# Performance work log

Hardware: AMD Instinct MI355X
Metric: run time of the kernel (lower is better)

The kernel has to match this reference:

```python
import jax, jax.numpy as jnp
from jax import lax
import numpy as np

B, T, C = 4, 1024, 1024
NH, HS = 16, 64
K, STRIDE = 32, 16
EPS = 1e-5


def _ln(x, w, b):
    m = jnp.mean(x, axis=-1, keepdims=True)
    v = jnp.mean((x - m) ** 2, axis=-1, keepdims=True)
    return (x - m) * lax.rsqrt(v + EPS) * w + b


def setup_inputs() -> dict:
    key = jax.random.key(0)
    ks = jax.random.split(key, 12)
    s = 0.02
    return {
        'x': jax.random.normal(ks[0], (B, T, C), jnp.float32),
        'c_attn_w': jax.random.normal(ks[1], (C, 3 * C), jnp.float32) * s,
        'c_attn_b': jnp.zeros((3 * C,), jnp.float32),
        'c_proj_w': jax.random.normal(ks[2], (C, C), jnp.float32) * s,
        'c_proj_b': jnp.zeros((C,), jnp.float32),
        'conv_w': jax.random.normal(ks[3], (HS, HS, K), jnp.float32) * s,  # OIH
        'conv_b': jnp.zeros((HS,), jnp.float32),
        'comp_ln_w': jnp.ones((HS,), jnp.float32),
        'comp_ln_b': jnp.zeros((HS,), jnp.float32),
        'ln_local_w': jnp.ones((C,), jnp.float32),
        'ln_local_b': jnp.zeros((C,), jnp.float32),
        'gate_w1': jax.random.normal(ks[4], (2 * C, C), jnp.float32) * s,
        'gate_b1': jnp.zeros((C,), jnp.float32),
        'gate_ln_w': jnp.ones((C,), jnp.float32),
        'gate_ln_b': jnp.zeros((C,), jnp.float32),
        'gate_w2': jax.random.normal(ks[5], (C, 2), jnp.float32) * s,
        'gate_b2': jnp.zeros((2,), jnp.float32),
    }


def _compress(h, conv_w, conv_b, comp_ln_w, comp_ln_b):
    # h: [B, nh, T, hs] -> [B, nh, num_blocks, hs]
    b, nh, t, hs = h.shape
    xr = h.transpose(0, 1, 3, 2).reshape(b * nh, hs, t)  # NCH
    co = lax.conv_general_dilated(xr, conv_w, (STRIDE,), 'VALID',
                                  dimension_numbers=('NCH', 'OIH', 'NCH'))
    co = co + conv_b[None, :, None]
    y = co.transpose(0, 2, 1)  # [B*nh, nb, hs]
    y = _ln(y, comp_ln_w, comp_ln_b)
    y = jax.nn.gelu(y, approximate=False)
    return y.reshape(b, nh, -1, hs)


def _attn(q, k, v, mask):
    # q:[B,nh,T,hs] k,v:[B,nh,Tk,hs], mask:[T,Tk] bool (True=keep)
    scale = 1.0 / jnp.sqrt(jnp.asarray(q.shape[-1], q.dtype))
    att = jnp.einsum('bhqd,bhkd->bhqk', q, k) * scale
    att = jnp.where(mask[None, None], att, jnp.finfo(att.dtype).min)
    att = jax.nn.softmax(att, axis=-1)
    return jnp.einsum('bhqk,bhkd->bhqd', att, v)


def reference(x, c_attn_w, c_attn_b, c_proj_w, c_proj_b, conv_w, conv_b,
              comp_ln_w, comp_ln_b, ln_local_w, ln_local_b,
              gate_w1, gate_b1, gate_ln_w, gate_ln_b, gate_w2, gate_b2):
    b, t, c = x.shape
    qkv = x @ c_attn_w + c_attn_b
    q, k, v = jnp.split(qkv, 3, axis=-1)
    q = q.reshape(b, t, NH, HS).transpose(0, 2, 1, 3)
    k = k.reshape(b, t, NH, HS).transpose(0, 2, 1, 3)
    v = v.reshape(b, t, NH, HS).transpose(0, 2, 1, 3)

    k_comp = _compress(k, conv_w, conv_b, comp_ln_w, comp_ln_b)
    v_comp = _compress(v, conv_w, conv_b, comp_ln_w, comp_ln_b)
    nb = k_comp.shape[2]

    # local branch: flash path with is_causal=True skips the window mask -> plain causal
    causal = jnp.tril(jnp.ones((t, t), bool))
    local = _attn(q, k, v, causal)
    local = local.transpose(0, 2, 1, 3).reshape(b, t, c)
    local_norm = _ln(local, ln_local_w, ln_local_b)

    # compressed branch: causal mask of shape [T, num_blocks], diagonal 0
    comp_mask = jnp.tril(jnp.ones((t, nb), bool), k=0)
    comp = _attn(q, k_comp, v_comp, comp_mask)
    comp = comp.transpose(0, 2, 1, 3).reshape(b, t, c)

    # gating from last-token features
    feats = jnp.concatenate([local_norm[:, -1, :], comp[:, -1, :]], axis=-1)  # [B, 2C]
    h = jax.nn.relu(_ln(feats @ gate_w1 + gate_b1, gate_ln_w, gate_ln_b))
    gates = jax.nn.softmax(h @ gate_w2 + gate_b2, axis=-1)  # [B, 2]
    g = gates[:, None, :]  # [B, 1, 2]
    combined = g[..., 0:1] * local_norm + g[..., 1:2] * comp

    return combined @ c_proj_w + c_proj_b
```

## Files before the change

### kernel.cpp

```cpp
#include <hip/hip_runtime.h>

using u16 = unsigned short;
using f32x4 = __attribute__((ext_vector_type(4))) float;
using s16x8 = __attribute__((ext_vector_type(8))) short;
using u16x4 = __attribute__((ext_vector_type(4))) unsigned short;

__device__ __forceinline__ u16 f2bf(float f) {
  unsigned u = __float_as_uint(f);
  return (u16)((u + 0x7FFFu + ((u >> 16) & 1u)) >> 16);
}

__device__ __forceinline__ f32x4 mfma16(s16x8 a, s16x8 b, f32x4 c) {
  return __builtin_amdgcn_mfma_f32_16x16x32_bf16(a, b, c, 0, 0, 0);
}

__device__ __forceinline__ void gld16(const void* g, void* l) {
  __builtin_amdgcn_global_load_lds(
      (const __attribute__((address_space(1))) unsigned int*)g,
      (__attribute__((address_space(3))) unsigned int*)l, 16, 0, 0);
}

__global__ __launch_bounds__(256) void cast_bf16(const float* __restrict__ in,
                                                 u16* __restrict__ out, int n4) {
  int i = blockIdx.x * 256 + threadIdx.x;
  if (i >= n4) return;
  f32x4 v = *(const f32x4*)(in + (size_t)i * 4);
  u16x4 o = {f2bf(v[0]), f2bf(v[1]), f2bf(v[2]), f2bf(v[3])};
  *(u16x4*)(out + (size_t)i * 4) = o;
}

__global__ __launch_bounds__(256) void cast_wfrag(const float* __restrict__ in,
                                                  u16* __restrict__ out) {
  int t = blockIdx.x * 256 + threadIdx.x;
  int c = t & 63, blk = t >> 6;
  int j = blk & 3, ic = blk >> 2;
  int lr = c >> 2, lg = c & 3;
  const float* src = in + (size_t)(j * 16 + lr) * 2048 + ic * 32 + lg * 8;
  f32x4 a = *(const f32x4*)(src);
  f32x4 b = *(const f32x4*)(src + 4);
  u16* dst = out + (size_t)t * 8;
  u16x4 o0 = {f2bf(a[0]), f2bf(a[1]), f2bf(a[2]), f2bf(a[3])};
  u16x4 o1 = {f2bf(b[0]), f2bf(b[1]), f2bf(b[2]), f2bf(b[3])};
  *(u16x4*)(dst) = o0;
  *(u16x4*)(dst + 4) = o1;
}

__global__ __launch_bounds__(256) void transpose_cast(const float* __restrict__ in,
                                                      u16* __restrict__ out,
                                                      int R, int C) {
  __shared__ float t[32][33];
  int bx = blockIdx.x, by = blockIdx.y;
  int tx = threadIdx.x & 31, ty = threadIdx.x >> 5;
#pragma unroll
  for (int r = 0; r < 4; r++) {
    int row = by * 32 + ty + r * 8;
    t[ty + r * 8][tx] = in[(size_t)row * C + bx * 32 + tx];
  }
  __syncthreads();
#pragma unroll
  for (int r = 0; r < 4; r++) {
    int orow = bx * 32 + ty + r * 8;
    out[(size_t)orow * R + by * 32 + tx] = f2bf(t[tx][ty + r * 8]);
  }
}

__device__ __forceinline__ void gemm_mainloop(const u16* A, const u16* Bt, int K,
                                              u16* As, u16* Bs, f32x4 acc[4][4]) {
  const int tid = threadIdx.x;
  const int row = tid >> 2, c16 = tid & 3;
  const int lane = tid & 63, wid = tid >> 6;
  const int wm = wid >> 1, wn = wid & 1, lg = lane >> 4, lr = lane & 15;
  const u16* ga = A + (size_t)row * K + c16 * 8;
  const u16* gb = Bt + (size_t)row * K + c16 * 8;
  const size_t rowskip = (size_t)64 * K;
  for (int k0 = 0; k0 < K; k0 += 32) {
    gld16(ga + k0, As + tid * 8);
    gld16(ga + rowskip + k0, As + 2048 + tid * 8);
    gld16(gb + k0, Bs + tid * 8);
    gld16(gb + rowskip + k0, Bs + 2048 + tid * 8);
    __syncthreads();
    s16x8 af[4], bfr[4];
#pragma unroll
    for (int i = 0; i < 4; i++)
      af[i] = *(const s16x8*)(As + (wm * 64 + i * 16 + lr) * 32 + lg * 8);
#pragma unroll
    for (int j = 0; j < 4; j++)
      bfr[j] = *(const s16x8*)(Bs + (wn * 64 + j * 16 + lr) * 32 + lg * 8);
#pragma unroll
    for (int i = 0; i < 4; i++)
#pragma unroll
      for (int j = 0; j < 4; j++) acc[i][j] = mfma16(af[i], bfr[j], acc[i][j]);
    __syncthreads();
  }
}

__global__ __launch_bounds__(256) void gemm_qkv(const u16* __restrict__ A,
                                                const u16* __restrict__ Bt,
                                                const float* __restrict__ bias,
                                                u16* __restrict__ qo, u16* __restrict__ ko,
                                                u16* __restrict__ kTo, u16* __restrict__ vTo) {
  __shared__ u16 As[4096];
  __shared__ u16 Bs[4096];
  int m0 = blockIdx.x * 128, n0 = blockIdx.y * 128;
  f32x4 acc[4][4] = {};
  gemm_mainloop(A + (size_t)m0 * 1024, Bt + (size_t)n0 * 1024, 1024, As, Bs, acc);
  int lane = threadIdx.x & 63, wid = threadIdx.x >> 6;
  int wm = wid >> 1, wn = wid & 1, lg = lane >> 4, lr = lane & 15;
#pragma unroll
  for (int i = 0; i < 4; i++) {
    int mb = m0 + wm * 64 + i * 16 + lg * 4;
    int b = mb >> 10, tb = mb & 1023;
#pragma unroll
    for (int j = 0; j < 4; j++) {
      int n = n0 + wn * 64 + j * 16 + lr;
      float bs = bias[n];
      int sel = n >> 10, hd = n & 1023, h = hd >> 6, d = hd & 63;
      int bh = b * 16 + h;
      u16 u0 = f2bf(acc[i][j][0] + bs), u1 = f2bf(acc[i][j][1] + bs);
      u16 u2 = f2bf(acc[i][j][2] + bs), u3 = f2bf(acc[i][j][3] + bs);
      if (sel == 0) {
        u16* qp = qo + ((size_t)bh << 16) + ((size_t)tb << 6) + d;
        qp[0] = u0; qp[64] = u1; qp[128] = u2; qp[192] = u3;
      } else if (sel == 1) {
        u16* kp = ko + ((size_t)bh << 16) + ((size_t)tb << 6) + d;
        kp[0] = u0; kp[64] = u1; kp[128] = u2; kp[192] = u3;
        u16x4 pk = {u0, u1, u2, u3};
        *(u16x4*)(kTo + ((size_t)(bh * 64 + d) << 10) + tb) = pk;
      } else {
        u16x4 pk = {u0, u1, u2, u3};
        *(u16x4*)(vTo + ((size_t)(bh * 64 + d) << 10) + tb) = pk;
      }
    }
  }
}

__global__ __launch_bounds__(256) void gemm_proj(const u16* __restrict__ A,
                                                 const u16* __restrict__ Bt,
                                                 const float* __restrict__ bias,
                                                 float* __restrict__ out) {
  __shared__ u16 As[4096];
  __shared__ u16 Bs[4096];
  int m0 = blockIdx.x * 128, n0 = blockIdx.y * 128;
  f32x4 acc[4][4] = {};
  gemm_mainloop(A + (size_t)m0 * 1024, Bt + (size_t)n0 * 1024, 1024, As, Bs, acc);
  int lane = threadIdx.x & 63, wid = threadIdx.x >> 6;
  int wm = wid >> 1, wn = wid & 1, lg = lane >> 4, lr = lane & 15;
#pragma unroll
  for (int i = 0; i < 4; i++) {
    int mb = m0 + wm * 64 + i * 16 + lg * 4;
#pragma unroll
    for (int j = 0; j < 4; j++) {
      int n = n0 + wn * 64 + j * 16 + lr;
      float bs = bias[n];
#pragma unroll
      for (int r = 0; r < 4; r++)
        out[(size_t)(mb + r) * 1024 + n] = acc[i][j][r] + bs;
    }
  }
}

__global__ __launch_bounds__(512, 2) void conv_comp(const u16* __restrict__ kT,
                                                    const u16* __restrict__ vT,
                                                    const u16* __restrict__ wfrag,
                                                    const float* __restrict__ cb,
                                                    const float* __restrict__ lnw,
                                                    const float* __restrict__ lnb,
                                                    u16* __restrict__ kcomp,
                                                    u16* __restrict__ vcompT) {
  __shared__ float red[4][64][16];
  int bh = blockIdx.x, sel = blockIdx.y;
  const u16* src = (sel ? vT : kT) + ((size_t)bh << 16);
  int tid = threadIdx.x, w = tid >> 6, lane = tid & 63, lg = lane >> 4, lr = lane & 15;
  int wq = w & 3, ichalf = w >> 2;
  f32x4 acc[4] = {};
  int arow = wq * 16 + lr;
  if (arow > 62) arow = 62;
  const u16* abase = src + (size_t)arow * 16 + lg * 8;
  const u16* wbase = wfrag + (size_t)(lr * 4 + lg) * 8;
  int ic0 = ichalf * 32;
#pragma unroll 8
  for (int ic = ic0; ic < ic0 + 32; ic++) {
    s16x8 a = *(const s16x8*)(abase + ic * 1024);
    const u16* wrow = wbase + (size_t)ic * 2048;
#pragma unroll
    for (int j = 0; j < 4; j++) {
      s16x8 bfr = *(const s16x8*)(wrow + j * 512);
      acc[j] = mfma16(a, bfr, acc[j]);
    }
  }
  if (w >= 4) {
#pragma unroll
    for (int j = 0; j < 4; j++)
#pragma unroll
      for (int r = 0; r < 4; r++) red[wq][lane][j * 4 + r] = acc[j][r];
  }
  __syncthreads();
  if (w >= 4) return;
#pragma unroll
  for (int j = 0; j < 4; j++)
#pragma unroll
    for (int r = 0; r < 4; r++) acc[j][r] += red[wq][lane][j * 4 + r];
  float lwv[4], lbv[4];
#pragma unroll
  for (int j = 0; j < 4; j++) {
    int oc = j * 16 + lr;
    float cbv = cb[oc];
    acc[j][0] += cbv; acc[j][1] += cbv; acc[j][2] += cbv; acc[j][3] += cbv;
    lwv[j] = lnw[oc]; lbv[j] = lnb[oc];
  }
#pragma unroll
  for (int r = 0; r < 4; r++) {
    float s = acc[0][r] + acc[1][r] + acc[2][r] + acc[3][r];
    float q = acc[0][r] * acc[0][r] + acc[1][r] * acc[1][r] +
              acc[2][r] * acc[2][r] + acc[3][r] * acc[3][r];
#pragma unroll
    for (int off = 1; off < 16; off <<= 1) {
      s += __shfl_xor(s, off);
      q += __shfl_xor(q, off);
    }
    float mean = s * (1.f / 64.f);
    float var = q * (1.f / 64.f) - mean * mean;
    float rstd = rsqrtf(fmaxf(var, 0.f) + 1e-5f);
    int op = wq * 16 + lg * 4 + r;
#pragma unroll
    for (int j = 0; j < 4; j++) {
      float y = (acc[j][r] - mean) * rstd * lwv[j] + lbv[j];
      y = 0.5f * y * (1.0f + erff(y * 0.70710678118f));
      if (op > 62) y = 0.f;
      int oc = j * 16 + lr;
      if (sel == 0) kcomp[((size_t)bh << 12) + (op << 6) + oc] = f2bf(y);
      else          vcompT[((size_t)bh << 12) + (oc << 6) + op] = f2bf(y);
    }
  }
}

__global__ __launch_bounds__(256, 4) void flash64(const u16* __restrict__ qg,
                                                  const u16* __restrict__ kg,
                                                  const u16* __restrict__ vg,
                                                  float* __restrict__ outg,
                                                  int k_bh, int v_bh, int vrow, int kvmax) {
  __shared__ u16 Ks[2][4096];
  __shared__ u16 Pl[4][1152];
  const int tid = threadIdx.x;
  const int w = tid >> 6, lane = tid & 63, lg = lane >> 4, lr = lane & 15;
  const int idx = blockIdx.x;
  const int nqt = gridDim.x >> 6;
  const int xcd = idx & 7, j = idx >> 3;
  const int bh = xcd * 8 + (j & 7);
  const int qt0 = nqt - 1 - (j >> 3);
  const int q0 = qt0 * 64;
  const int qrow = q0 + w * 16 + lr;
  const u16* qb = qg + ((size_t)bh << 16) + (size_t)qrow * 64 + lg * 8;
  s16x8 qf0 = *(const s16x8*)(qb);
  s16x8 qf1 = *(const s16x8*)(qb + 32);
  const u16* kb = kg + (size_t)bh * k_bh;
  const u16* vb = vg + (size_t)bh * v_bh;
  int nt = qt0 + 1;
  int ntk = (kvmax + 63) >> 6;
  if (nt > ntk) nt = ntk;
  u16* Pw = Pl[w];
  f32x4 ot[4] = {};
  float m = -INFINITY, l = 0.f;
  const float SCL = 0.125f * 1.44269504089f;

  auto stageK = [&](int bufi, int kv0) {
#pragma unroll
    for (int rnd = 0; rnd < 2; rnd++) {
      int o = tid * 16 + rnd * 4096;
      int row = o >> 7;
      int sb = (o & 127) ^ ((row & 7) << 4);
      gld16(kb + (size_t)(kv0 + row) * 64 + (sb >> 1), &Ks[bufi][o >> 1]);
    }
  };

  stageK(0, 0);
  int cur = 0;
  for (int t = 0; t < nt; t++) {
    __syncthreads();
    if (t + 1 < nt) stageK(cur ^ 1, (t + 1) * 64);
    const int kv0 = t * 64;
    const u16* Kb = Ks[cur];
    const bool full = (kv0 + 63 <= q0 + w * 16) && (kv0 + 64 <= kvmax);
    s16x8 vlo[4];
#pragma unroll
    for (int d4 = 0; d4 < 4; d4++)
      vlo[d4] = *(const s16x8*)(vb + (size_t)(d4 * 16 + lr) * vrow + kv0 + lg * 8);
    f32x4 st[4];
    __builtin_amdgcn_s_setprio(1);
#pragma unroll
    for (int kvt = 0; kvt < 4; kvt++) {
      int rr = kvt * 16 + lr;
      int sw = (rr & 7) << 4;
      s16x8 k0 = *(const s16x8*)(Kb + (((rr << 7) + ((lg * 16) ^ sw)) >> 1));
      s16x8 k1 = *(const s16x8*)(Kb + (((rr << 7) + ((64 + lg * 16) ^ sw)) >> 1));
      f32x4 z = {};
      z = mfma16(k0, qf0, z);
      z = mfma16(k1, qf1, z);
      st[kvt] = z;
    }
    __builtin_amdgcn_s_setprio(0);
    s16x8 vhi[4];
#pragma unroll
    for (int d4 = 0; d4 < 4; d4++)
      vhi[d4] = *(const s16x8*)(vb + (size_t)(d4 * 16 + lr) * vrow + kv0 + 32 + lg * 8);
    float p[16];
    float tm = -INFINITY;
    if (full) {
#pragma unroll
      for (int kvt = 0; kvt < 4; kvt++)
#pragma unroll
        for (int r = 0; r < 4; r++) {
          float v = st[kvt][r] * SCL;
          p[kvt * 4 + r] = v;
          tm = fmaxf(tm, v);
        }
    } else {
#pragma unroll
      for (int kvt = 0; kvt < 4; kvt++)
#pragma unroll
        for (int r = 0; r < 4; r++) {
          int kvi = kv0 + kvt * 16 + lg * 4 + r;
          float v = st[kvt][r] * SCL;
          v = (kvi <= qrow && kvi < kvmax) ? v : -INFINITY;
          p[kvt * 4 + r] = v;
          tm = fmaxf(tm, v);
        }
    }
    tm = fmaxf(tm, __shfl_xor(tm, 16));
    tm = fmaxf(tm, __shfl_xor(tm, 32));
    if (!__all(tm <= m)) {
      float mnew = fmaxf(m, tm);
      float fac = exp2f(m - mnew);
      l *= fac;
#pragma unroll
      for (int d4 = 0; d4 < 4; d4++) {
        ot[d4][0] *= fac; ot[d4][1] *= fac; ot[d4][2] *= fac; ot[d4][3] *= fac;
      }
      m = mnew;
    }
    float ls = 0.f;
#pragma unroll
    for (int i = 0; i < 16; i++) {
      float e = exp2f(p[i] - m);
      p[i] = e;
      ls += e;
    }
    ls += __shfl_xor(ls, 16);
    ls += __shfl_xor(ls, 32);
    l += ls;
#pragma unroll
    for (int kvt = 0; kvt < 4; kvt++) {
      unsigned w0 = (unsigned)f2bf(p[kvt * 4 + 0]) | ((unsigned)f2bf(p[kvt * 4 + 1]) << 16);
      unsigned w1 = (unsigned)f2bf(p[kvt * 4 + 2]) | ((unsigned)f2bf(p[kvt * 4 + 3]) << 16);
      uint2 pk = {w0, w1};
      *(uint2*)(Pw + lr * 72 + kvt * 16 + lg * 4) = pk;
    }
    s16x8 bp0 = *(const s16x8*)(Pw + lr * 72 + lg * 8);
    s16x8 bp1 = *(const s16x8*)(Pw + lr * 72 + 32 + lg * 8);
    __builtin_amdgcn_s_setprio(1);
#pragma unroll
    for (int d4 = 0; d4 < 4; d4++) {
      ot[d4] = mfma16(vlo[d4], bp0, ot[d4]);
      ot[d4] = mfma16(vhi[d4], bp1, ot[d4]);
    }
    __builtin_amdgcn_s_setprio(0);
    cur ^= 1;
  }
  float inv = 1.f / l;
  int b = bh >> 4, h = bh & 15;
  float* op = outg + ((size_t)((b << 10) + qrow) << 10) + h * 64;
#pragma unroll
  for (int d4 = 0; d4 < 4; d4++) {
    f32x4 v;
#pragma unroll
    for (int c = 0; c < 4; c++) v[c] = ot[d4][c] * inv;
    *(f32x4*)(op + d4 * 16 + lg * 4) = v;
  }
}

__global__ __launch_bounds__(256) void ln_rows(float* __restrict__ x,
                                               const float* __restrict__ w,
                                               const float* __restrict__ b) {
  __shared__ float red[8];
  size_t row = blockIdx.x;
  float* xr = x + (row << 10);
  int tid = threadIdx.x;
  f32x4 v = *(const f32x4*)(xr + tid * 4);
  float s = v[0] + v[1] + v[2] + v[3];
  float q = v[0] * v[0] + v[1] * v[1] + v[2] * v[2] + v[3] * v[3];
#pragma unroll
  for (int off = 32; off >= 1; off >>= 1) {
    s += __shfl_xor(s, off);
    q += __shfl_xor(q, off);
  }
  int wid = tid >> 6;
  if ((tid & 63) == 0) { red[wid * 2] = s; red[wid * 2 + 1] = q; }
  __syncthreads();
  s = red[0] + red[2] + red[4] + red[6];
  q = red[1] + red[3] + red[5] + red[7];
  float mean = s * (1.0f / 1024.0f);
  float var = q * (1.0f / 1024.0f) - mean * mean;
  float rstd = rsqrtf(fmaxf(var, 0.f) + 1e-5f);
  f32x4 wv = *(const f32x4*)(w + tid * 4);
  f32x4 bv = *(const f32x4*)(b + tid * 4);
  f32x4 o;
#pragma unroll
  for (int c = 0; c < 4; c++) o[c] = (v[c] - mean) * rstd * wv[c] + bv[c];
  *(f32x4*)(xr + tid * 4) = o;
}

__global__ __launch_bounds__(256) void gate_partial(const float* __restrict__ ln,
                                                    const float* __restrict__ comp,
                                                    const float* __restrict__ w1,
                                                    float* __restrict__ partial) {
  __shared__ float f[4][32];
  int ib = blockIdx.x, i0 = ib * 32, tid = threadIdx.x;
  if (tid < 128) {
    int bb = tid >> 5, ii = tid & 31;
    int i = i0 + ii;
    const float* src = (i < 1024) ? ln : comp;
    int ic = i & 1023;
    f[bb][ii] = src[((size_t)(bb * 1024 + 1023) << 10) + ic];
  }
  __syncthreads();
  float acc[4][4] = {};
  for (int ii = 0; ii < 32; ii++) {
    float f0 = f[0][ii], f1 = f[1][ii], f2 = f[2][ii], f3 = f[3][ii];
#pragma unroll
    for (int jj = 0; jj < 4; jj++) {
      float w = w1[(size_t)(i0 + ii) * 1024 + jj * 256 + tid];
      acc[jj][0] += f0 * w; acc[jj][1] += f1 * w;
      acc[jj][2] += f2 * w; acc[jj][3] += f3 * w;
    }
  }
#pragma unroll
  for (int jj = 0; jj < 4; jj++)
#pragma unroll
    for (int bb = 0; bb < 4; bb++)
      partial[(size_t)((ib << 2) + bb) * 1024 + jj * 256 + tid] = acc[jj][bb];
}

__global__ __launch_bounds__(1024) void gate_finish(const float* __restrict__ partial,
                                                    const float* __restrict__ b1,
                                                    const float* __restrict__ lnw,
                                                    const float* __restrict__ lnb,
                                                    const float* __restrict__ w2,
                                                    const float* __restrict__ b2,
                                                    float* __restrict__ g) {
  __shared__ float redA[16], redB[16];
  int b = blockIdx.x, j = threadIdx.x;
  float s = b1[j];
#pragma unroll 4
  for (int ib = 0; ib < 64; ib++) s += partial[(size_t)((ib << 2) + b) * 1024 + j];
  float sa = s, sb = s * s;
#pragma unroll
  for (int off = 32; off >= 1; off >>= 1) {
    sa += __shfl_xor(sa, off);
    sb += __shfl_xor(sb, off);
  }
  int wid = j >> 6;
  if ((j & 63) == 0) { redA[wid] = sa; redB[wid] = sb; }
  __syncthreads();
  if (j == 0) {
    float A = 0, Bv = 0;
    for (int k2 = 0; k2 < 16; k2++) { A += redA[k2]; Bv += redB[k2]; }
    redA[0] = A; redB[0] = Bv;
  }
  __syncthreads();
  float S = redA[0], Q = redB[0];
  float mean = S * (1.f / 1024.f), var = Q * (1.f / 1024.f) - mean * mean;
  float rstd = rsqrtf(fmaxf(var, 0.f) + 1e-5f);
  float hn = (s - mean) * rstd * lnw[j] + lnb[j];
  hn = fmaxf(hn, 0.f);
  float c0 = hn * w2[j * 2], c1 = hn * w2[j * 2 + 1];
  __syncthreads();
  float ra = c0, rb = c1;
#pragma unroll
  for (int off = 32; off >= 1; off >>= 1) {
    ra += __shfl_xor(ra, off);
    rb += __shfl_xor(rb, off);
  }
  if ((j & 63) == 0) { redA[wid] = ra; redB[wid] = rb; }
  __syncthreads();
  if (j == 0) {
    float A = 0, Bv = 0;
    for (int k2 = 0; k2 < 16; k2++) { A += redA[k2]; Bv += redB[k2]; }
    A += b2[0]; Bv += b2[1];
    float mx = fmaxf(A, Bv);
    float e0 = __expf(A - mx), e1 = __expf(Bv - mx);
    float inv = 1.f / (e0 + e1);
    g[b * 2] = e0 * inv;
    g[b * 2 + 1] = e1 * inv;
  }
}

__global__ __launch_bounds__(256) void combine_k(const float* __restrict__ ln,
                                                 const float* __restrict__ comp,
                                                 const float* __restrict__ g,
                                                 u16* __restrict__ out) {
  size_t i = (size_t)blockIdx.x * 256 + threadIdx.x;
  size_t off = i << 2;
  int b = (int)(off >> 20);
  float g0 = g[b * 2], g1 = g[b * 2 + 1];
  f32x4 a = *(const f32x4*)(ln + off);
  f32x4 c = *(const f32x4*)(comp + off);
  u16x4 o = {f2bf(g0 * a[0] + g1 * c[0]), f2bf(g0 * a[1] + g1 * c[1]),
             f2bf(g0 * a[2] + g1 * c[2]), f2bf(g0 * a[3] + g1 * c[3])};
  *(u16x4*)(out + off) = o;
}

extern "C" void kernel_launch(void* const* d_in, const int* in_sizes, int n_in,
                              void* d_out, int out_size, void* d_ws, size_t ws_size,
                              hipStream_t stream) {
  const float* x        = (const float*)d_in[0];
  const float* c_attn_w = (const float*)d_in[1];
  const float* c_attn_b = (const float*)d_in[2];
  const float* c_proj_w = (const float*)d_in[3];
  const float* c_proj_b = (const float*)d_in[4];
  const float* conv_w   = (const float*)d_in[5];
  const float* conv_b   = (const float*)d_in[6];
  const float* comp_ln_w= (const float*)d_in[7];
  const float* comp_ln_b= (const float*)d_in[8];
  const float* ln_loc_w = (const float*)d_in[9];
  const float* ln_loc_b = (const float*)d_in[10];
  const float* gate_w1  = (const float*)d_in[11];
  const float* gate_b1  = (const float*)d_in[12];
  const float* gate_ln_w= (const float*)d_in[13];
  const float* gate_ln_b= (const float*)d_in[14];
  const float* gate_w2  = (const float*)d_in[15];
  const float* gate_b2  = (const float*)d_in[16];
  float* out = (float*)d_out;

  char* ws = (char*)d_ws;
  size_t off = 0;
  auto alloc = [&](size_t bytes) -> char* {
    char* p = ws + off;
    off += (bytes + 255) & ~(size_t)255;
    return p;
  };
  u16* x_bf     = (u16*)alloc(8388608);
  u16* attn_wT  = (u16*)alloc(6291456);
  u16* proj_wT  = (u16*)alloc(2097152);
  u16* wfrag    = (u16*)alloc(262144);
  u16* q_bf     = (u16*)alloc(8388608);
  u16* k_bf     = (u16*)alloc(8388608);
  u16* kT_bf    = (u16*)alloc(8388608);
  u16* vT_bf    = (u16*)alloc(8388608);
  u16* k_comp   = (u16*)alloc(524288);
  u16* v_compT  = (u16*)alloc(524288);
  float* local  = (float*)alloc(16777216);
  float* comp   = (float*)alloc(16777216);
  float* partial= (float*)alloc(1048576);
  float* gbuf   = (float*)alloc(256);
  u16* combined = x_bf;
  if (off > ws_size) return;

  cast_bf16<<<dim3(4096), dim3(256), 0, stream>>>(x, x_bf, 1048576);
  transpose_cast<<<dim3(96, 32), dim3(256), 0, stream>>>(c_attn_w, attn_wT, 1024, 3072);
  transpose_cast<<<dim3(32, 32), dim3(256), 0, stream>>>(c_proj_w, proj_wT, 1024, 1024);
  cast_wfrag<<<dim3(64), dim3(256), 0, stream>>>(conv_w, wfrag);

  gemm_qkv<<<dim3(32, 24), dim3(256), 0, stream>>>(x_bf, attn_wT, c_attn_b,
                                                   q_bf, k_bf, kT_bf, vT_bf);

  conv_comp<<<dim3(64, 2), dim3(512), 0, stream>>>(kT_bf, vT_bf, wfrag, conv_b,
                                                   comp_ln_w, comp_ln_b, k_comp, v_compT);

  flash64<<<dim3(1024), dim3(256), 0, stream>>>(q_bf, k_bf, vT_bf, local,
                                                65536, 65536, 1024, 1024);
  flash64<<<dim3(1024), dim3(256), 0, stream>>>(q_bf, k_comp, v_compT, comp,
                                                4096, 4096, 64, 63);

  ln_rows<<<dim3(4096), dim3(256), 0, stream>>>(local, ln_loc_w, ln_loc_b);

  gate_partial<<<dim3(64), dim3(256), 0, stream>>>(local, comp, gate_w1, partial);
  gate_finish<<<dim3(4), dim3(1024), 0, stream>>>(partial, gate_b1, gate_ln_w,
                                                  gate_ln_b, gate_w2, gate_b2, gbuf);

  combine_k<<<dim3(4096), dim3(256), 0, stream>>>(local, comp, gbuf, combined);
  gemm_proj<<<dim3(32, 8), dim3(256), 0, stream>>>(combined, proj_wT, c_proj_b, out);
}
```

Before: 279.6 us.

## Double-buffer LDS tiles in GEMM mainloop to overlap loads with MFMA

Gives the shared GEMM mainloop two LDS buffers for A and B. The next k-tile's global_load_lds is issued right after the barrier, before the current tile is consumed, and the second barrier per iteration is removed. MFMA issue priority is raised with s_setprio around the compute block. This is meant to hide global-load latency behind the matrix math, at the cost of doubled LDS use per block, which may lower occupancy.

```diff
diff --git a/kernel.cpp b/kernel.cpp
--- a/kernel.cpp
+++ b/kernel.cpp
@@ -65,7 +65,8 @@
 }
 
 __device__ __forceinline__ void gemm_mainloop(const u16* A, const u16* Bt, int K,
-                                              u16* As, u16* Bs, f32x4 acc[4][4]) {
+                                              u16 As[2][4096], u16 Bs[2][4096],
+                                              f32x4 acc[4][4]) {
   const int tid = threadIdx.x;
   const int row = tid >> 2, c16 = tid & 3;
   const int lane = tid & 63, wid = tid >> 6;
@@ -73,24 +74,35 @@
   const u16* ga = A + (size_t)row * K + c16 * 8;
   const u16* gb = Bt + (size_t)row * K + c16 * 8;
   const size_t rowskip = (size_t)64 * K;
+
+  auto stage = [&](int b, int k0) {
+    gld16(ga + k0, As[b] + tid * 8);
+    gld16(ga + rowskip + k0, As[b] + 2048 + tid * 8);
+    gld16(gb + k0, Bs[b] + tid * 8);
+    gld16(gb + rowskip + k0, Bs[b] + 2048 + tid * 8);
+  };
+
+  stage(0, 0);
+  int cur = 0;
   for (int k0 = 0; k0 < K; k0 += 32) {
-    gld16(ga + k0, As + tid * 8);
-    gld16(ga + rowskip + k0, As + 2048 + tid * 8);
-    gld16(gb + k0, Bs + tid * 8);
-    gld16(gb + rowskip + k0, Bs + 2048 + tid * 8);
     __syncthreads();
+    if (k0 + 32 < K) stage(cur ^ 1, k0 + 32);
+    const u16* Ab = As[cur];
+    const u16* Bb = Bs[cur];
     s16x8 af[4], bfr[4];
 #pragma unroll
     for (int i = 0; i < 4; i++)
-      af[i] = *(const s16x8*)(As + (wm * 64 + i * 16 + lr) * 32 + lg * 8);
+      af[i] = *(const s16x8*)(Ab + (wm * 64 + i * 16 + lr) * 32 + lg * 8);
 #pragma unroll
     for (int j = 0; j < 4; j++)
-      bfr[j] = *(const s16x8*)(Bs + (wn * 64 + j * 16 + lr) * 32 + lg * 8);
+      bfr[j] = *(const s16x8*)(Bb + (wn * 64 + j * 16 + lr) * 32 + lg * 8);
+    __builtin_amdgcn_s_setprio(1);
 #pragma unroll
     for (int i = 0; i < 4; i++)
 #pragma unroll
       for (int j = 0; j < 4; j++) acc[i][j] = mfma16(af[i], bfr[j], acc[i][j]);
-    __syncthreads();
+    __builtin_amdgcn_s_setprio(0);
+    cur ^= 1;
   }
 }
 
@@ -99,8 +111,8 @@
                                                 const float* __restrict__ bias,
                                                 u16* __restrict__ qo, u16* __restrict__ ko,
                                                 u16* __restrict__ kTo, u16* __restrict__ vTo) {
-  __shared__ u16 As[4096];
-  __shared__ u16 Bs[4096];
+  __shared__ u16 As[2][4096];
+  __shared__ u16 Bs[2][4096];
   int m0 = blockIdx.x * 128, n0 = blockIdx.y * 128;
   f32x4 acc[4][4] = {};
   gemm_mainloop(A + (size_t)m0 * 1024, Bt + (size_t)n0 * 1024, 1024, As, Bs, acc);
@@ -138,8 +150,8 @@
                                                  const u16* __restrict__ Bt,
                                                  const float* __restrict__ bias,
                                                  float* __restrict__ out) {
-  __shared__ u16 As[4096];
-  __shared__ u16 Bs[4096];
+  __shared__ u16 As[2][4096];
+  __shared__ u16 Bs[2][4096];
   int m0 = blockIdx.x * 128, n0 = blockIdx.y * 128;
   f32x4 acc[4][4] = {};
   gemm_mainloop(A + (size_t)m0 * 1024, Bt + (size_t)n0 * 1024, 1024, As, Bs, acc);
```

Result: no change. 280.5 us (+0.3%).
